# Kernel optimization log

Hardware: AMD Instinct MI355X
Metric: run time of the kernel (lower is better)

Reference implementation:

```python
import jax, jax.numpy as jnp
import numpy as np

EMBEDDING_DIM = 10
FEATURE_AMOUNT = 23
KQ_DIM = 10


def setup_inputs() -> dict:
    key = jax.random.key(0)
    k0, k1, k2, k3 = jax.random.split(key, 4)
    B = 262144
    inp = jax.random.normal(k0, (B, FEATURE_AMOUNT, EMBEDDING_DIM), dtype=jnp.float32)
    # torch nn.Linear weights stored as [out_features, in_features]
    Wk = jax.random.normal(k1, (KQ_DIM, EMBEDDING_DIM), dtype=jnp.float32) * 0.1
    Wq = jax.random.normal(k2, (KQ_DIM, EMBEDDING_DIM), dtype=jnp.float32) * 0.1
    Wv = jax.random.normal(k3, (EMBEDDING_DIM, EMBEDDING_DIM), dtype=jnp.float32) * 0.1
    return {"input": inp, "Wk": Wk, "Wq": Wq, "Wv": Wv}


def reference(input, Wk, Wq, Wv):
    # keys/querys/values: x @ W.T  (torch Linear, no bias)
    keys = jnp.einsum('bsd,kd->bsk', input, Wk)
    querys = jnp.einsum('bsd,kd->bsk', input, Wq)
    values = jnp.einsum('bsd,ed->bse', input, Wv)
    scale = 1.0 / np.sqrt(KQ_DIM).astype(np.float32)
    logits = jnp.einsum('bik,bjk->bij', querys, keys) * scale
    omega = jax.nn.softmax(logits, axis=-1)
    context = jnp.einsum('bij,bje->bie', omega, values)
    out = input + context
    return out.reshape(-1, FEATURE_AMOUNT * EMBEDDING_DIM)
```

## Files before the change

kernel.cpp:

```cpp
#include <hip/hip_runtime.h>
#include <hip/hip_fp16.h>

#define SEQ 23
#define DIM 10
#define BPB 11
#define NTHR 256

typedef _Float16 hf2 __attribute__((ext_vector_type(2)));

static __device__ __forceinline__ float fdot2(hf2 a, hf2 b, float c) {
#if __has_builtin(__builtin_amdgcn_fdot2)
    return __builtin_amdgcn_fdot2(a, b, c, false);
#else
    return c + (float)a[0] * (float)b[0] + (float)a[1] * (float)b[1];
#endif
}

static __device__ __forceinline__ unsigned pack2(float a, float b) {
    __half2 h = __floats2half2_rn(a, b);
    return __builtin_bit_cast(unsigned, h);
}
static __device__ __forceinline__ hf2 u2h(unsigned u) {
    return __builtin_bit_cast(hf2, u);
}
static __device__ __forceinline__ __half2 u2hh(unsigned u) {
    return __builtin_bit_cast(__half2, u);
}

__global__ void attn_prep_kernel(const float* __restrict__ Wk,
                                 const float* __restrict__ Wq,
                                 const float* __restrict__ Wv,
                                 unsigned* __restrict__ ws) {
    const int t = threadIdx.x;
    if (t < 50) {
        const int a = t / 5, p = t % 5;
        float m0 = 0.f, m1 = 0.f;
        #pragma unroll
        for (int k = 0; k < 10; ++k) {
            m0 += Wq[k * 10 + a] * Wk[k * 10 + 2 * p];
            m1 += Wq[k * 10 + a] * Wk[k * 10 + 2 * p + 1];
        }
        const float sc = 0.31622776601683794f;
        ws[t] = pack2(m0 * sc, m1 * sc);
    } else if (t < 100) {
        const int e = (t - 50) / 5, p = (t - 50) % 5;
        ws[t] = pack2(Wv[e * 10 + 2 * p], Wv[e * 10 + 2 * p + 1]);
    }
}

__global__ __launch_bounds__(NTHR) void attn_main_kernel(
    const float* __restrict__ x,
    const unsigned* __restrict__ wsu,
    float* __restrict__ out,
    int B)
{
    __shared__ __align__(16) unsigned ub2[BPB][SEQ][8];
    __shared__ __align__(16) unsigned vb2[BPB][SEQ][8];

    const int tid = threadIdx.x;
    const int bl  = tid / SEQ;
    const int i   = tid - bl * SEQ;
    const long b  = (long)blockIdx.x * BPB + bl;
    const bool act = (tid < BPB * SEQ) && (b < (long)B);

    float xr[DIM];
    hf2   xp[5];

    if (act) {
        const float* xpr = x + (b * SEQ + i) * DIM;
        #pragma unroll
        for (int p = 0; p < 5; ++p) {
            float2 t = *reinterpret_cast<const float2*>(xpr + 2 * p);
            xr[2 * p] = t.x; xr[2 * p + 1] = t.y;
            xp[p] = u2h(pack2(t.x, t.y));
        }
        unsigned urow[5], vrow[5];
        #pragma unroll
        for (int q = 0; q < 5; ++q) {
            float u0 = 0.f, u1 = 0.f, v0 = 0.f, v1 = 0.f;
            #pragma unroll
            for (int p = 0; p < 5; ++p) {
                u0 = fdot2(xp[p], u2h(wsu[(2 * q)     * 5 + p]), u0);
                u1 = fdot2(xp[p], u2h(wsu[(2 * q + 1) * 5 + p]), u1);
                v0 = fdot2(xp[p], u2h(wsu[50 + (2 * q)     * 5 + p]), v0);
                v1 = fdot2(xp[p], u2h(wsu[50 + (2 * q + 1) * 5 + p]), v1);
            }
            urow[q] = pack2(u0, u1);
            vrow[q] = pack2(v0, v1);
        }
        *reinterpret_cast<uint4*>(&ub2[bl][i][0]) =
            make_uint4(urow[0], urow[1], urow[2], urow[3]);
        ub2[bl][i][4] = urow[4];
        *reinterpret_cast<uint4*>(&vb2[bl][i][0]) =
            make_uint4(vrow[0], vrow[1], vrow[2], vrow[3]);
        vb2[bl][i][4] = vrow[4];
    }
    __syncthreads();
    if (!act) return;

    float s[SEQ];
    #pragma unroll
    for (int j = 0; j < SEQ; ++j) {
        const unsigned* r = &ub2[bl][j][0];
        uint4 r03 = *reinterpret_cast<const uint4*>(r);
        unsigned r4 = r[4];
        float acc = 0.f;
        acc = fdot2(xp[0], u2h(r03.x), acc);
        acc = fdot2(xp[1], u2h(r03.y), acc);
        acc = fdot2(xp[2], u2h(r03.z), acc);
        acc = fdot2(xp[3], u2h(r03.w), acc);
        acc = fdot2(xp[4], u2h(r4),    acc);
        s[j] = acc;
    }

    float m = s[0];
    #pragma unroll
    for (int j = 1; j < SEQ; ++j) m = fmaxf(m, s[j]);
    float sum = 0.f;
    #pragma unroll
    for (int j = 0; j < SEQ; ++j) { s[j] = __expf(s[j] - m); sum += s[j]; }
    const float inv = __builtin_amdgcn_rcpf(sum);

    __half2 c2[5];
    #pragma unroll
    for (int q = 0; q < 5; ++q) c2[q] = __float2half2_rn(0.f);
    #pragma unroll
    for (int j = 0; j < SEQ; ++j) {
        const unsigned* r = &vb2[bl][j][0];
        uint4 r03 = *reinterpret_cast<const uint4*>(r);
        unsigned r4 = r[4];
        __half2 ph = __float2half2_rn(s[j] * inv);
        c2[0] = __hfma2(ph, u2hh(r03.x), c2[0]);
        c2[1] = __hfma2(ph, u2hh(r03.y), c2[1]);
        c2[2] = __hfma2(ph, u2hh(r03.z), c2[2]);
        c2[3] = __hfma2(ph, u2hh(r03.w), c2[3]);
        c2[4] = __hfma2(ph, u2hh(r4),    c2[4]);
    }

    float* op = out + b * (SEQ * DIM) + i * DIM;
    #pragma unroll
    for (int q = 0; q < 5; ++q) {
        float2 cf = __half22float2(c2[q]);
        float2 t;
        t.x = xr[2 * q]     + cf.x;
        t.y = xr[2 * q + 1] + cf.y;
        *reinterpret_cast<float2*>(op + 2 * q) = t;
    }
}

extern "C" void kernel_launch(void* const* d_in, const int* in_sizes, int n_in,
                              void* d_out, int out_size, void* d_ws, size_t ws_size,
                              hipStream_t stream) {
    const float* x  = (const float*)d_in[0];
    const float* Wk = (const float*)d_in[1];
    const float* Wq = (const float*)d_in[2];
    const float* Wv = (const float*)d_in[3];
    float* out = (float*)d_out;
    unsigned* ws = (unsigned*)d_ws;

    const int B = in_sizes[0] / (SEQ * DIM);
    hipLaunchKernelGGL(attn_prep_kernel, dim3(1), dim3(128), 0, stream,
                       Wk, Wq, Wv, ws);
    const int blocks = (B + BPB - 1) / BPB;
    hipLaunchKernelGGL(attn_main_kernel, dim3(blocks), dim3(NTHR), 0, stream,
                       x, ws, out, B);
}
```

Before: 132.9 us.

## Attend over raw x in shared memory and apply Wv after softmax, two rows per thread

Shared memory now stores only the fp16 input rows. Each query row is pre-multiplied by the combined Wq^T Wk matrix, and the value projection moves after the softmax-weighted sum of raw x rows, so the separate K and V tiles disappear. Each thread handles two query rows, giving 21 batches per block and better reuse of the shared loads. The scale now folds in log2(e) so exp2 can be used, normalisation is deferred to the end, and launch bounds ask for 4 blocks. This raises register pressure and accumulates unnormalised weights in fp16, which risks overflow or precision loss.

```diff
diff --git a/kernel.cpp b/kernel.cpp
--- a/kernel.cpp
+++ b/kernel.cpp
@@ -3,8 +3,10 @@
 
 #define SEQ 23
 #define DIM 10
-#define BPB 11
+#define TPB 12
+#define BPB 21
 #define NTHR 256
+#define NROW (BPB * SEQ)
 
 typedef _Float16 hf2 __attribute__((ext_vector_type(2)));
 
@@ -15,7 +17,13 @@
     return c + (float)a[0] * (float)b[0] + (float)a[1] * (float)b[1];
 #endif
 }
-
+static __device__ __forceinline__ float fastexp2(float x) {
+#if __has_builtin(__builtin_amdgcn_exp2f)
+    return __builtin_amdgcn_exp2f(x);
+#else
+    return exp2f(x);
+#endif
+}
 static __device__ __forceinline__ unsigned pack2(float a, float b) {
     __half2 h = __floats2half2_rn(a, b);
     return __builtin_bit_cast(unsigned, h);
@@ -25,6 +33,9 @@
 }
 static __device__ __forceinline__ __half2 u2hh(unsigned u) {
     return __builtin_bit_cast(__half2, u);
+}
+static __device__ __forceinline__ hf2 h2f(__half2 h) {
+    return __builtin_bit_cast(hf2, h);
 }
 
 __global__ void attn_prep_kernel(const float* __restrict__ Wk,
@@ -37,10 +48,10 @@
         float m0 = 0.f, m1 = 0.f;
         #pragma unroll
         for (int k = 0; k < 10; ++k) {
-            m0 += Wq[k * 10 + a] * Wk[k * 10 + 2 * p];
-            m1 += Wq[k * 10 + a] * Wk[k * 10 + 2 * p + 1];
-        }
-        const float sc = 0.31622776601683794f;
+            m0 += Wq[k * 10 + 2 * p]     * Wk[k * 10 + a];
+            m1 += Wq[k * 10 + 2 * p + 1] * Wk[k * 10 + a];
+        }
+        const float sc = 0.31622776601683794f * 1.44269504088896340f;
         ws[t] = pack2(m0 * sc, m1 * sc);
     } else if (t < 100) {
         const int e = (t - 50) / 5, p = (t - 50) % 5;
@@ -48,103 +59,159 @@
     }
 }
 
-__global__ __launch_bounds__(NTHR) void attn_main_kernel(
+__global__ __launch_bounds__(NTHR, 4) void attn_main_kernel(
     const float* __restrict__ x,
     const unsigned* __restrict__ wsu,
     float* __restrict__ out,
     int B)
 {
-    __shared__ __align__(16) unsigned ub2[BPB][SEQ][8];
-    __shared__ __align__(16) unsigned vb2[BPB][SEQ][8];
+    __shared__ __align__(16) unsigned xb[NROW + 1][8];
 
     const int tid = threadIdx.x;
-    const int bl  = tid / SEQ;
-    const int i   = tid - bl * SEQ;
+    const int bl  = tid / TPB;
+    const int t   = tid - bl * TPB;
     const long b  = (long)blockIdx.x * BPB + bl;
-    const bool act = (tid < BPB * SEQ) && (b < (long)B);
-
-    float xr[DIM];
-    hf2   xp[5];
+    const bool act  = (tid < BPB * TPB) && (b < (long)B);
+    const bool hasB = act && (t < TPB - 1);
+
+    const int rA = t, rB = t + TPB;
+
+    float xrA[DIM], xrB[DIM];
+    hf2   xpA[5], xpB[5];
+    unsigned upA[5], upB[5];
 
     if (act) {
-        const float* xpr = x + (b * SEQ + i) * DIM;
+        const float* pa = x + (b * SEQ + rA) * DIM;
+        const float* pb = x + (b * SEQ + (hasB ? rB : rA)) * DIM;
         #pragma unroll
         for (int p = 0; p < 5; ++p) {
-            float2 t = *reinterpret_cast<const float2*>(xpr + 2 * p);
-            xr[2 * p] = t.x; xr[2 * p + 1] = t.y;
-            xp[p] = u2h(pack2(t.x, t.y));
-        }
-        unsigned urow[5], vrow[5];
+            float2 ta = *reinterpret_cast<const float2*>(pa + 2 * p);
+            float2 tb = *reinterpret_cast<const float2*>(pb + 2 * p);
+            xrA[2 * p] = ta.x; xrA[2 * p + 1] = ta.y;
+            xrB[2 * p] = tb.x; xrB[2 * p + 1] = tb.y;
+            xpA[p] = u2h(pack2(ta.x, ta.y));
+            xpB[p] = u2h(pack2(tb.x, tb.y));
+        }
+        const int rowA = bl * SEQ + rA;
+        const int rowB = hasB ? (bl * SEQ + rB) : NROW;
+        *reinterpret_cast<uint4*>(&xb[rowA][0]) = make_uint4(
+            __builtin_bit_cast(unsigned, xpA[0]), __builtin_bit_cast(unsigned, xpA[1]),
+            __builtin_bit_cast(unsigned, xpA[2]), __builtin_bit_cast(unsigned, xpA[3]));
+        xb[rowA][4] = __builtin_bit_cast(unsigned, xpA[4]);
+        *reinterpret_cast<uint4*>(&xb[rowB][0]) = make_uint4(
+            __builtin_bit_cast(unsigned, xpB[0]), __builtin_bit_cast(unsigned, xpB[1]),
+            __builtin_bit_cast(unsigned, xpB[2]), __builtin_bit_cast(unsigned, xpB[3]));
+        xb[rowB][4] = __builtin_bit_cast(unsigned, xpB[4]);
+
         #pragma unroll
         for (int q = 0; q < 5; ++q) {
-            float u0 = 0.f, u1 = 0.f, v0 = 0.f, v1 = 0.f;
+            float a0 = 0.f, a1 = 0.f, b0 = 0.f, b1 = 0.f;
             #pragma unroll
             for (int p = 0; p < 5; ++p) {
-                u0 = fdot2(xp[p], u2h(wsu[(2 * q)     * 5 + p]), u0);
-                u1 = fdot2(xp[p], u2h(wsu[(2 * q + 1) * 5 + p]), u1);
-                v0 = fdot2(xp[p], u2h(wsu[50 + (2 * q)     * 5 + p]), v0);
-                v1 = fdot2(xp[p], u2h(wsu[50 + (2 * q + 1) * 5 + p]), v1);
+                const hf2 m0 = u2h(wsu[(2 * q) * 5 + p]);
+                const hf2 m1 = u2h(wsu[(2 * q + 1) * 5 + p]);
+                a0 = fdot2(xpA[p], m0, a0);
+                a1 = fdot2(xpA[p], m1, a1);
+                b0 = fdot2(xpB[p], m0, b0);
+                b1 = fdot2(xpB[p], m1, b1);
             }
-            urow[q] = pack2(u0, u1);
-            vrow[q] = pack2(v0, v1);
-        }
-        *reinterpret_cast<uint4*>(&ub2[bl][i][0]) =
-            make_uint4(urow[0], urow[1], urow[2], urow[3]);
-        ub2[bl][i][4] = urow[4];
-        *reinterpret_cast<uint4*>(&vb2[bl][i][0]) =
-            make_uint4(vrow[0], vrow[1], vrow[2], vrow[3]);
-        vb2[bl][i][4] = vrow[4];
+            upA[q] = pack2(a0, a1);
+            upB[q] = pack2(b0, b1);
+        }
     }
     __syncthreads();
     if (!act) return;
 
-    float s[SEQ];
+    const unsigned (*xrow)[8] = &xb[bl * SEQ];
+
+    float sA[SEQ], sB[SEQ];
     #pragma unroll
     for (int j = 0; j < SEQ; ++j) {
-        const unsigned* r = &ub2[bl][j][0];
-        uint4 r03 = *reinterpret_cast<const uint4*>(r);
-        unsigned r4 = r[4];
-        float acc = 0.f;
-        acc = fdot2(xp[0], u2h(r03.x), acc);
-        acc = fdot2(xp[1], u2h(r03.y), acc);
-        acc = fdot2(xp[2], u2h(r03.z), acc);
-        acc = fdot2(xp[3], u2h(r03.w), acc);
-        acc = fdot2(xp[4], u2h(r4),    acc);
-        s[j] = acc;
-    }
-
-    float m = s[0];
-    #pragma unroll
-    for (int j = 1; j < SEQ; ++j) m = fmaxf(m, s[j]);
-    float sum = 0.f;
-    #pragma unroll
-    for (int j = 0; j < SEQ; ++j) { s[j] = __expf(s[j] - m); sum += s[j]; }
-    const float inv = __builtin_amdgcn_rcpf(sum);
-
-    __half2 c2[5];
-    #pragma unroll
-    for (int q = 0; q < 5; ++q) c2[q] = __float2half2_rn(0.f);
+        uint4 q4 = *reinterpret_cast<const uint4*>(&xrow[j][0]);
+        unsigned q1 = xrow[j][4];
+        float a = fdot2(u2h(upA[0]), u2h(q4.x), 0.f);
+        a = fdot2(u2h(upA[1]), u2h(q4.y), a);
+        a = fdot2(u2h(upA[2]), u2h(q4.z), a);
+        a = fdot2(u2h(upA[3]), u2h(q4.w), a);
+        a = fdot2(u2h(upA[4]), u2h(q1),   a);
+        sA[j] = a;
+        float c = fdot2(u2h(upB[0]), u2h(q4.x), 0.f);
+        c = fdot2(u2h(upB[1]), u2h(q4.y), c);
+        c = fdot2(u2h(upB[2]), u2h(q4.z), c);
+        c = fdot2(u2h(upB[3]), u2h(q4.w), c);
+        c = fdot2(u2h(upB[4]), u2h(q1),   c);
+        sB[j] = c;
+    }
+
+#define F3(a, b, c) fmaxf(fmaxf((a), (b)), (c))
+    float mA, mB;
+    {
+        const float t0 = F3(sA[0], sA[1], sA[2]),   t1 = F3(sA[3], sA[4], sA[5]);
+        const float t2 = F3(sA[6], sA[7], sA[8]),   t3 = F3(sA[9], sA[10], sA[11]);
+        const float t4 = F3(sA[12], sA[13], sA[14]), t5 = F3(sA[15], sA[16], sA[17]);
+        const float t6 = F3(sA[18], sA[19], sA[20]), t7 = fmaxf(sA[21], sA[22]);
+        mA = F3(F3(t0, t1, t2), F3(t3, t4, t5), fmaxf(t6, t7));
+    }
+    {
+        const float t0 = F3(sB[0], sB[1], sB[2]),   t1 = F3(sB[3], sB[4], sB[5]);
+        const float t2 = F3(sB[6], sB[7], sB[8]),   t3 = F3(sB[9], sB[10], sB[11]);
+        const float t4 = F3(sB[12], sB[13], sB[14]), t5 = F3(sB[15], sB[16], sB[17]);
+        const float t6 = F3(sB[18], sB[19], sB[20]), t7 = fmaxf(sB[21], sB[22]);
+        mB = F3(F3(t0, t1, t2), F3(t3, t4, t5), fmaxf(t6, t7));
+    }
+
+    __half2 wA[5], wB[5];
+    #pragma unroll
+    for (int q = 0; q < 5; ++q) { wA[q] = __float2half2_rn(0.f); wB[q] = __float2half2_rn(0.f); }
+    float smA0 = 0.f, smA1 = 0.f, smB0 = 0.f, smB1 = 0.f;
+
     #pragma unroll
     for (int j = 0; j < SEQ; ++j) {
-        const unsigned* r = &vb2[bl][j][0];
-        uint4 r03 = *reinterpret_cast<const uint4*>(r);
-        unsigned r4 = r[4];
-        __half2 ph = __float2half2_rn(s[j] * inv);
-        c2[0] = __hfma2(ph, u2hh(r03.x), c2[0]);
-        c2[1] = __hfma2(ph, u2hh(r03.y), c2[1]);
-        c2[2] = __hfma2(ph, u2hh(r03.z), c2[2]);
-        c2[3] = __hfma2(ph, u2hh(r03.w), c2[3]);
-        c2[4] = __hfma2(ph, u2hh(r4),    c2[4]);
-    }
-
-    float* op = out + b * (SEQ * DIM) + i * DIM;
+        uint4 q4 = *reinterpret_cast<const uint4*>(&xrow[j][0]);
+        unsigned q1 = xrow[j][4];
+        const float pA = fastexp2(sA[j] - mA);
+        const float pB = fastexp2(sB[j] - mB);
+        if (j & 1) { smA1 += pA; smB1 += pB; } else { smA0 += pA; smB0 += pB; }
+        const __half2 hA = __float2half2_rn(pA);
+        const __half2 hB = __float2half2_rn(pB);
+        wA[0] = __hfma2(hA, u2hh(q4.x), wA[0]);
+        wA[1] = __hfma2(hA, u2hh(q4.y), wA[1]);
+        wA[2] = __hfma2(hA, u2hh(q4.z), wA[2]);
+        wA[3] = __hfma2(hA, u2hh(q4.w), wA[3]);
+        wA[4] = __hfma2(hA, u2hh(q1),   wA[4]);
+        wB[0] = __hfma2(hB, u2hh(q4.x), wB[0]);
+        wB[1] = __hfma2(hB, u2hh(q4.y), wB[1]);
+        wB[2] = __hfma2(hB, u2hh(q4.z), wB[2]);
+        wB[3] = __hfma2(hB, u2hh(q4.w), wB[3]);
+        wB[4] = __hfma2(hB, u2hh(q1),   wB[4]);
+    }
+
+    const float invA = __builtin_amdgcn_rcpf(smA0 + smA1);
+    const float invB = __builtin_amdgcn_rcpf(smB0 + smB1);
+
+    float* opA = out + (b * SEQ + rA) * DIM;
+    float* opB = out + (b * SEQ + rB) * DIM;
     #pragma unroll
     for (int q = 0; q < 5; ++q) {
-        float2 cf = __half22float2(c2[q]);
-        float2 t;
-        t.x = xr[2 * q]     + cf.x;
-        t.y = xr[2 * q + 1] + cf.y;
-        *reinterpret_cast<float2*>(op + 2 * q) = t;
+        float e0A = 0.f, e1A = 0.f, e0B = 0.f, e1B = 0.f;
+        #pragma unroll
+        for (int p = 0; p < 5; ++p) {
+            const hf2 v0 = u2h(wsu[50 + (2 * q) * 5 + p]);
+            const hf2 v1 = u2h(wsu[50 + (2 * q + 1) * 5 + p]);
+            e0A = fdot2(h2f(wA[p]), v0, e0A);
+            e1A = fdot2(h2f(wA[p]), v1, e1A);
+            e0B = fdot2(h2f(wB[p]), v0, e0B);
+            e1B = fdot2(h2f(wB[p]), v1, e1B);
+        }
+        float2 oa, ob;
+        oa.x = fmaf(e0A, invA, xrA[2 * q]);
+        oa.y = fmaf(e1A, invA, xrA[2 * q + 1]);
+        *reinterpret_cast<float2*>(opA + 2 * q) = oa;
+        if (hasB) {
+            ob.x = fmaf(e0B, invB, xrB[2 * q]);
+            ob.y = fmaf(e1B, invB, xrB[2 * q + 1]);
+            *reinterpret_cast<float2*>(opB + 2 * q) = ob;
+        }
     }
 }
 
```

Measured after the change: 476.2 us. +258.4%, slower.
